# Optimization experiments

Hardware: AMD Instinct MI355X
Metric: run time of the kernel (lower is better)

## Reference

```python
import jax, jax.numpy as jnp
import numpy as np

# Mamba2 defaults (mamba_ssm): expand=2, headdim=64, d_conv=4, ngroups=1
D_MODEL, D_STATE, D_INNER, HEADDIM, D_CONV = 512, 64, 1024, 64, 4
NHEADS = D_INNER // HEADDIM  # 16
CONV_DIM = D_INNER + 2 * D_STATE  # 1152
D_IN_PROJ = 2 * D_INNER + 2 * D_STATE + NHEADS  # 2192
BATCH, SEQLEN = 2, 2048
RMS_EPS = 1.1920929e-07  # torch nn.RMSNorm eps=None -> fp32 machine eps
GNORM_EPS = 1e-5  # mamba_ssm RMSNormGated default


def _rms(t, w, eps):
    return t * jax.lax.rsqrt(jnp.mean(t * t, axis=-1, keepdims=True) + eps) * w


def _mamba2(u, in_w, conv_w, conv_b, dt_bias, A_log, Dp, gnorm_w, out_w):
    """Mamba2 block forward (ngroups=1). u: (b, l, d_model) -> (b, l, d_model)."""
    b, l, _ = u.shape
    zxbcdt = jnp.einsum('bld,ed->ble', u, in_w)  # (b, l, 2192)
    z = zxbcdt[..., :D_INNER]
    xBC = zxbcdt[..., D_INNER:D_INNER + CONV_DIM]
    dt = jax.nn.softplus(zxbcdt[..., -NHEADS:] + dt_bias)  # (b, l, h)
    # causal depthwise conv, kernel D_CONV, then SiLU
    xp = jnp.pad(xBC, ((0, 0), (D_CONV - 1, 0), (0, 0)))
    xBC = conv_b + sum(xp[:, i:i + l, :] * conv_w[:, i] for i in range(D_CONV))
    xBC = jax.nn.silu(xBC)
    x = xBC[..., :D_INNER].reshape(b, l, NHEADS, HEADDIM)
    Bm = xBC[..., D_INNER:D_INNER + D_STATE]  # (b, l, n)
    Cm = xBC[..., D_INNER + D_STATE:]         # (b, l, n)
    dA = jnp.exp(dt * (-jnp.exp(A_log)))      # (b, l, h), decay per head

    def step(h, inp):
        dA_t, dt_t, B_t, C_t, x_t = inp  # (b,h) (b,h) (b,n) (b,n) (b,h,p)
        h = h * dA_t[:, :, None, None] + jnp.einsum('bh,bhp,bn->bhpn', dt_t, x_t, B_t)
        y = jnp.einsum('bhpn,bn->bhp', h, C_t)
        return h, y

    h0 = jnp.zeros((b, NHEADS, HEADDIM, D_STATE), u.dtype)
    xs = (jnp.swapaxes(dA, 0, 1), jnp.swapaxes(dt, 0, 1), jnp.swapaxes(Bm, 0, 1),
          jnp.swapaxes(Cm, 0, 1), jnp.swapaxes(x, 0, 1))
    _, ys = jax.lax.scan(step, h0, xs)  # (l, b, h, p)
    y = jnp.swapaxes(ys, 0, 1) + x * Dp[None, None, :, None]
    y = y.reshape(b, l, D_INNER)
    # gated RMSNorm: norm(y * silu(z)) * weight
    y = y * jax.nn.silu(z)
    y = _rms(y, gnorm_w, GNORM_EPS)
    return jnp.einsum('bli,oi->blo', y, out_w)


def _layer(x, pos_emb, pixel_mask, norm_ssm_w, norm_ffn_w, ffn_w1, ffn_b1, ffn_w2, ffn_b2,
           f_in_w, f_conv_w, f_conv_b, f_dt_bias, f_A_log, f_D, f_gnorm_w, f_out_w,
           b_in_w, b_conv_w, b_conv_b, b_dt_bias, b_A_log, b_D, b_gnorm_w, b_out_w):
    si = _rms(x, norm_ssm_w, RMS_EPS) + pos_emb
    fwd = _mamba2(si, f_in_w, f_conv_w, f_conv_b, f_dt_bias, f_A_log, f_D, f_gnorm_w, f_out_w)
    bwd = jnp.flip(_mamba2(jnp.flip(si, 1), b_in_w, b_conv_w, b_conv_b, b_dt_bias,
                           b_A_log, b_D, b_gnorm_w, b_out_w), 1)
    ssm_out = (fwd + bwd) * pixel_mask[..., None]  # merge='add'
    x = x + ssm_out
    h = _rms(x, norm_ffn_w, RMS_EPS)
    h = jax.nn.gelu(h @ ffn_w1.T + ffn_b1, approximate=False)
    return x + (h @ ffn_w2.T + ffn_b2)


def setup_inputs() -> dict:
    key = jax.random.key(0)
    ks = jax.random.split(key, 16)
    f32 = jnp.float32
    inp = {}
    inp['x'] = jax.random.normal(ks[0], (BATCH, SEQLEN, D_MODEL), f32)
    inp['pos_emb'] = jax.random.normal(ks[1], (BATCH, SEQLEN, D_MODEL), f32) * 0.02
    inp['pixel_mask'] = jnp.ones((BATCH, SEQLEN), f32)
    inp['norm_ssm_w'] = jnp.ones((D_MODEL,), f32)
    inp['norm_ffn_w'] = jnp.ones((D_MODEL,), f32)
    d_ffn = 4 * D_MODEL
    inp['ffn_w1'] = jax.random.normal(ks[2], (d_ffn, D_MODEL), f32) * 0.02
    inp['ffn_b1'] = jnp.zeros((d_ffn,), f32)
    inp['ffn_w2'] = jax.random.normal(ks[3], (D_MODEL, d_ffn), f32) * 0.02
    inp['ffn_b2'] = jnp.zeros((D_MODEL,), f32)
    i = 4
    for pre in ('f', 'b'):
        inp[pre + '_in_w'] = jax.random.normal(ks[i], (D_IN_PROJ, D_MODEL), f32) * 0.02; i += 1
        inp[pre + '_conv_w'] = jax.random.uniform(ks[i], (CONV_DIM, D_CONV), f32, -0.5, 0.5); i += 1
        inp[pre + '_conv_b'] = jnp.zeros((CONV_DIM,), f32)
        dt0 = jnp.exp(jax.random.uniform(ks[i], (NHEADS,), f32) * (jnp.log(0.1) - jnp.log(0.001)) + jnp.log(0.001)); i += 1
        inp[pre + '_dt_bias'] = dt0 + jnp.log(-jnp.expm1(-dt0))  # inverse softplus
        inp[pre + '_A_log'] = jnp.log(jax.random.uniform(ks[i], (NHEADS,), f32, 1.0, 16.0)); i += 1
        inp[pre + '_D'] = jnp.ones((NHEADS,), f32)
        inp[pre + '_gnorm_w'] = jnp.ones((D_INNER,), f32)
        inp[pre + '_out_w'] = jax.random.normal(ks[i], (D_MODEL, D_INNER), f32) * 0.02; i += 1
    return inp


def reference(x, pos_emb, pixel_mask, norm_ssm_w, norm_ffn_w, ffn_w1, ffn_b1, ffn_w2, ffn_b2,
              f_in_w, f_conv_w, f_conv_b, f_dt_bias, f_A_log, f_D, f_gnorm_w, f_out_w,
              b_in_w, b_conv_w, b_conv_b, b_dt_bias, b_A_log, b_D, b_gnorm_w, b_out_w):
    return _layer(x, pos_emb, pixel_mask, norm_ssm_w, norm_ffn_w, ffn_w1, ffn_b1, ffn_w2, ffn_b2,
                  f_in_w, f_conv_w, f_conv_b, f_dt_bias, f_A_log, f_D, f_gnorm_w, f_out_w,
                  b_in_w, b_conv_w, b_conv_b, b_dt_bias, b_A_log, b_D, b_gnorm_w, b_out_w)
```

## Files before the change

### kernel.cpp

```cpp
#include <hip/hip_runtime.h>
#include <hip/hip_bf16.h>

typedef unsigned short u16;
typedef unsigned int u32;
typedef __bf16 bf16x8 __attribute__((ext_vector_type(8)));
typedef float f32x4 __attribute__((ext_vector_type(4)));

typedef __attribute__((address_space(1))) void gvoid_t;
typedef __attribute__((address_space(3))) void lvoid_t;
__device__ __forceinline__ void lds_cp16(void* lds, const void* g) {
    __builtin_amdgcn_global_load_lds((gvoid_t*)g, (lvoid_t*)lds, 16, 0, 0);
}

__device__ __forceinline__ float bf2f(u16 v) {
    u32 x = (u32)v << 16;
    return __builtin_bit_cast(float, x);
}
__device__ __forceinline__ u16 f2bf(float f) {
    return __builtin_bit_cast(u16, (__bf16)f);
}

__device__ __forceinline__ float wave_sum(float v) {
    #pragma unroll
    for (int o = 32; o > 0; o >>= 1) v += __shfl_xor(v, o);
    return v;
}

__device__ __forceinline__ void cvt4(const float* __restrict__ s, u16* __restrict__ d) {
    float4 v = *(const float4*)s;
    ushort4 o;
    o.x = f2bf(v.x); o.y = f2bf(v.y); o.z = f2bf(v.z); o.w = f2bf(v.w);
    *(ushort4*)d = o;
}

__global__ __launch_bounds__(256) void k_prep(
    const float* __restrict__ f_inw, const float* __restrict__ b_inw,
    const float* __restrict__ f_ow, const float* __restrict__ b_ow,
    const float* __restrict__ w1, const float* __restrict__ w2,
    u16* __restrict__ INWF, u16* __restrict__ INWB,
    u16* __restrict__ OWF, u16* __restrict__ OWB,
    u16* __restrict__ W1B, u16* __restrict__ W2B,
    const float* __restrict__ x, const float* __restrict__ pe,
    const float* __restrict__ wrms, u16* __restrict__ sib) {
    if (blockIdx.x < 5376) {
        int g = blockIdx.x * 256 + threadIdx.x;
        if (g < 294912) {
            int i = g * 4, n = i >> 9;
            if (n < 2192) cvt4(f_inw + i, INWF + i);
            else *(ushort4*)(INWF + i) = make_ushort4(0, 0, 0, 0);
            return;
        }
        g -= 294912;
        if (g < 294912) {
            int i = g * 4, n = i >> 9;
            if (n < 2192) cvt4(b_inw + i, INWB + i);
            else *(ushort4*)(INWB + i) = make_ushort4(0, 0, 0, 0);
            return;
        }
        g -= 294912;
        if (g < 131072) { cvt4(f_ow + g * 4, OWF + g * 4); return; }
        g -= 131072;
        if (g < 131072) { cvt4(b_ow + g * 4, OWB + g * 4); return; }
        g -= 131072;
        if (g < 262144) { cvt4(w1 + g * 4, W1B + g * 4); return; }
        g -= 262144;
        cvt4(w2 + g * 4, W2B + g * 4);
        return;
    }
    int row = (blockIdx.x - 5376) * 4 + (threadIdx.x >> 6);
    int lane = threadIdx.x & 63;
    size_t base = (size_t)row * 512 + lane * 4;
    float4 xa = *(const float4*)(x + base);
    float4 xb = *(const float4*)(x + base + 256);
    float ss = xa.x * xa.x + xa.y * xa.y + xa.z * xa.z + xa.w * xa.w
             + xb.x * xb.x + xb.y * xb.y + xb.z * xb.z + xb.w * xb.w;
    ss = wave_sum(ss);
    float sc = rsqrtf(ss * (1.f / 512.f) + 1.1920929e-07f);
    float4 pa = *(const float4*)(pe + base);
    float4 pb = *(const float4*)(pe + base + 256);
    float4 wa = *(const float4*)(wrms + lane * 4);
    float4 wb = *(const float4*)(wrms + lane * 4 + 256);
    ushort4 oa, obv;
    oa.x = f2bf(xa.x * sc * wa.x + pa.x);
    oa.y = f2bf(xa.y * sc * wa.y + pa.y);
    oa.z = f2bf(xa.z * sc * wa.z + pa.z);
    oa.w = f2bf(xa.w * sc * wa.w + pa.w);
    obv.x = f2bf(xb.x * sc * wb.x + pb.x);
    obv.y = f2bf(xb.y * sc * wb.y + pb.y);
    obv.z = f2bf(xb.z * sc * wb.z + pb.z);
    obv.w = f2bf(xb.w * sc * wb.w + pb.w);
    *(ushort4*)(sib + base) = oa;
    *(ushort4*)(sib + base + 256) = obv;
}

__global__ __launch_bounds__(256) void k_gemm_in(
    const u16* __restrict__ A, const u16* __restrict__ W0, const u16* __restrict__ W1,
    u16* __restrict__ Z0, u16* __restrict__ Z1,
    u16* __restrict__ XB0, u16* __restrict__ XB1) {
    const int z = blockIdx.z;
    const u16* W = z ? W1 : W0;
    u16* Z = z ? Z1 : Z0;
    u16* XB = z ? XB1 : XB0;
    const int K = 512;

    __shared__ __align__(16) u16 As[2][128 * 32];
    __shared__ __align__(16) u16 Bs[2][128 * 32];

    const int t = threadIdx.x;
    const int lane = t & 63;
    const int w = t >> 6;
    const int m0 = blockIdx.y * 128;
    const int n0 = blockIdx.x * 128;
    const int wm = (w >> 1) * 64;
    const int wn = (w & 1) * 64;
    const int fr = lane & 15;
    const int ksw = (((lane >> 4) ^ ((fr >> 1) & 3)) & 3) * 8;

    f32x4 acc[4][4];
    #pragma unroll
    for (int i = 0; i < 4; ++i)
        #pragma unroll
        for (int j = 0; j < 4; ++j) acc[i][j] = (f32x4){0.f, 0.f, 0.f, 0.f};

    auto STAGE = [&](int buf, int kt) {
        #pragma unroll
        for (int j = 0; j < 2; ++j) {
            int off16 = j * 256 + t;
            int row = off16 >> 2;
            int kc = (((off16 & 3) ^ ((row >> 1) & 3)) & 3) * 8;
            int gm = m0 + row;
            if (z) gm = (gm & ~2047) | (2047 - (gm & 2047));
            lds_cp16(As[buf] + off16 * 8, A + (size_t)gm * K + kt + kc);
            lds_cp16(Bs[buf] + off16 * 8, W + (size_t)(n0 + row) * K + kt + kc);
        }
    };

    STAGE(0, 0);
    __syncthreads();
    int cur = 0;
    for (int kt = 0; kt < K; kt += 32) {
        if (kt + 32 < K) STAGE(cur ^ 1, kt + 32);
        bf16x8 af[4], bfr[4];
        #pragma unroll
        for (int i = 0; i < 4; ++i) af[i] = *(const bf16x8*)(As[cur] + (wm + i * 16 + fr) * 32 + ksw);
        #pragma unroll
        for (int i = 0; i < 4; ++i) bfr[i] = *(const bf16x8*)(Bs[cur] + (wn + i * 16 + fr) * 32 + ksw);
        #pragma unroll
        for (int i = 0; i < 4; ++i)
            #pragma unroll
            for (int j = 0; j < 4; ++j)
                acc[i][j] = __builtin_amdgcn_mfma_f32_16x16x32_bf16(af[i], bfr[j], acc[i][j], 0, 0, 0);
        __syncthreads();
        cur ^= 1;
    }
    #pragma unroll
    for (int i = 0; i < 4; ++i) {
        int rbase = m0 + wm + i * 16 + (lane >> 4) * 4;
        #pragma unroll
        for (int j = 0; j < 4; ++j) {
            int c = n0 + wn + j * 16 + fr;
            #pragma unroll
            for (int r = 0; r < 4; ++r) {
                u16 v = f2bf(acc[i][j][r]);
                int m = rbase + r;
                if (c < 1024) Z[(size_t)m * 1024 + c] = v;
                else if (c < 2192) XB[(size_t)m * 1184 + (c - 1024)] = v;
            }
        }
    }
}

template <int EPI>
__global__ __launch_bounds__(256) void k_gemm128(
    const u16* __restrict__ A0, const u16* __restrict__ A1,
    const u16* __restrict__ W0, const u16* __restrict__ W1,
    u16* __restrict__ C0, u16* __restrict__ C1, int N, int K,
    const float* __restrict__ bias, const float* __restrict__ resid,
    float* __restrict__ outf) {
    const int z = blockIdx.z;
    const u16* A = z ? A1 : A0;
    const u16* W = z ? W1 : W0;
    u16* C = z ? C1 : C0;

    __shared__ __align__(16) u16 As[2][128 * 32];
    __shared__ __align__(16) u16 Bs[2][128 * 32];

    const int t = threadIdx.x;
    const int lane = t & 63;
    const int w = t >> 6;
    const int m0 = blockIdx.y * 128;
    const int n0 = blockIdx.x * 128;
    const int wm = (w >> 1) * 64;
    const int wn = (w & 1) * 64;
    const int fr = lane & 15;
    const int ksw = (((lane >> 4) ^ ((fr >> 1) & 3)) & 3) * 8;

    f32x4 acc[4][4];
    #pragma unroll
    for (int i = 0; i < 4; ++i)
        #pragma unroll
        for (int j = 0; j < 4; ++j) acc[i][j] = (f32x4){0.f, 0.f, 0.f, 0.f};

    auto STAGE = [&](int buf, int kt) {
        #pragma unroll
        for (int j = 0; j < 2; ++j) {
            int off16 = j * 256 + t;
            int row = off16 >> 2;
            int kc = (((off16 & 3) ^ ((row >> 1) & 3)) & 3) * 8;
            lds_cp16(As[buf] + off16 * 8, A + (size_t)(m0 + row) * K + kt + kc);
            lds_cp16(Bs[buf] + off16 * 8, W + (size_t)(n0 + row) * K + kt + kc);
        }
    };

    STAGE(0, 0);
    __syncthreads();
    int cur = 0;
    for (int kt = 0; kt < K; kt += 32) {
        if (kt + 32 < K) STAGE(cur ^ 1, kt + 32);
        bf16x8 af[4], bfr[4];
        #pragma unroll
        for (int i = 0; i < 4; ++i) af[i] = *(const bf16x8*)(As[cur] + (wm + i * 16 + fr) * 32 + ksw);
        #pragma unroll
        for (int i = 0; i < 4; ++i) bfr[i] = *(const bf16x8*)(Bs[cur] + (wn + i * 16 + fr) * 32 + ksw);
        #pragma unroll
        for (int i = 0; i < 4; ++i)
            #pragma unroll
            for (int j = 0; j < 4; ++j)
                acc[i][j] = __builtin_amdgcn_mfma_f32_16x16x32_bf16(af[i], bfr[j], acc[i][j], 0, 0, 0);
        __syncthreads();
        cur ^= 1;
    }
    #pragma unroll
    for (int i = 0; i < 4; ++i) {
        int rbase = m0 + wm + i * 16 + (lane >> 4) * 4;
        #pragma unroll
        for (int j = 0; j < 4; ++j) {
            int col = n0 + wn + j * 16 + fr;
            #pragma unroll
            for (int r = 0; r < 4; ++r) {
                int m = rbase + r;
                float v = acc[i][j][r];
                if (EPI == 0) {
                    C[(size_t)m * N + col] = f2bf(v);
                } else if (EPI == 1) {
                    float xg = v + bias[col];
                    C[(size_t)m * N + col] = f2bf(0.5f * xg * (1.f + erff(xg * 0.70710678118654752f)));
                } else {
                    outf[(size_t)m * N + col] = v + bias[col] + resid[(size_t)m * N + col];
                }
            }
        }
    }
}

template <int EPI>
__global__ __launch_bounds__(256) void k_gemm12864(
    const u16* __restrict__ A0, const u16* __restrict__ A1,
    const u16* __restrict__ W0, const u16* __restrict__ W1,
    u16* __restrict__ C0, u16* __restrict__ C1, int N, int K,
    const float* __restrict__ bias, const float* __restrict__ resid,
    float* __restrict__ outf) {
    const int z = blockIdx.z;
    const u16* A = z ? A1 : A0;
    const u16* W = z ? W1 : W0;
    u16* C = z ? C1 : C0;

    __shared__ __align__(16) u16 As[2][128 * 32];
    __shared__ __align__(16) u16 Bs[2][64 * 32];

    const int t = threadIdx.x;
    const int lane = t & 63;
    const int w = t >> 6;
    const int m0 = blockIdx.y * 128;
    const int n0 = blockIdx.x * 64;
    const int wm = w * 32;
    const int fr = lane & 15;
    const int ksw = (((lane >> 4) ^ ((fr >> 1) & 3)) & 3) * 8;

    f32x4 acc[2][4];
    #pragma unroll
    for (int i = 0; i < 2; ++i)
        #pragma unroll
        for (int j = 0; j < 4; ++j) acc[i][j] = (f32x4){0.f, 0.f, 0.f, 0.f};

    auto STAGE = [&](int buf, int kt) {
        #pragma unroll
        for (int j = 0; j < 2; ++j) {
            int off16 = j * 256 + t;
            int row = off16 >> 2;
            int kc = (((off16 & 3) ^ ((row >> 1) & 3)) & 3) * 8;
            lds_cp16(As[buf] + off16 * 8, A + (size_t)(m0 + row) * K + kt + kc);
        }
        int brow = t >> 2;
        int bkc = (((t & 3) ^ ((brow >> 1) & 3)) & 3) * 8;
        lds_cp16(Bs[buf] + t * 8, W + (size_t)(n0 + brow) * K + kt + bkc);
    };

    STAGE(0, 0);
    __syncthreads();
    int cur = 0;
    for (int kt = 0; kt < K; kt += 32) {
        if (kt + 32 < K) STAGE(cur ^ 1, kt + 32);
        bf16x8 af[2], bfr[4];
        #pragma unroll
        for (int i = 0; i < 2; ++i) af[i] = *(const bf16x8*)(As[cur] + (wm + i * 16 + fr) * 32 + ksw);
        #pragma unroll
        for (int j = 0; j < 4; ++j) bfr[j] = *(const bf16x8*)(Bs[cur] + (j * 16 + fr) * 32 + ksw);
        #pragma unroll
        for (int i = 0; i < 2; ++i)
            #pragma unroll
            for (int j = 0; j < 4; ++j)
                acc[i][j] = __builtin_amdgcn_mfma_f32_16x16x32_bf16(af[i], bfr[j], acc[i][j], 0, 0, 0);
        __syncthreads();
        cur ^= 1;
    }
    #pragma unroll
    for (int i = 0; i < 2; ++i) {
        int rbase = m0 + wm + i * 16 + (lane >> 4) * 4;
        #pragma unroll
        for (int j = 0; j < 4; ++j) {
            int col = n0 + j * 16 + fr;
            #pragma unroll
            for (int r = 0; r < 4; ++r) {
                int m = rbase + r;
                float v = acc[i][j][r];
                if (EPI == 0) {
                    C[(size_t)m * N + col] = f2bf(v);
                } else if (EPI == 1) {
                    float xg = v + bias[col];
                    C[(size_t)m * N + col] = f2bf(0.5f * xg * (1.f + erff(xg * 0.70710678118654752f)));
                } else {
                    outf[(size_t)m * N + col] = v + bias[col] + resid[(size_t)m * N + col];
                }
            }
        }
    }
}

template <int EPI>
__global__ __launch_bounds__(256) void k_gemm64(
    const u16* __restrict__ A0, const u16* __restrict__ A1,
    const u16* __restrict__ W0, const u16* __restrict__ W1,
    u16* __restrict__ C0, u16* __restrict__ C1, int N, int K,
    const float* __restrict__ bias, const float* __restrict__ resid,
    float* __restrict__ outf) {
    const int z = blockIdx.z;
    const u16* A = z ? A1 : A0;
    const u16* W = z ? W1 : W0;
    u16* C = z ? C1 : C0;

    __shared__ __align__(16) u16 As[2][64 * 32];
    __shared__ __align__(16) u16 Bs[2][64 * 32];

    const int t = threadIdx.x;
    const int lane = t & 63;
    const int w = t >> 6;
    const int m0 = blockIdx.y * 64;
    const int n0 = blockIdx.x * 64;
    const int wm = (w >> 1) * 32;
    const int wn = (w & 1) * 32;
    const int fr = lane & 15;
    const int ksw = (((lane >> 4) ^ ((fr >> 1) & 3)) & 3) * 8;

    f32x4 acc[2][2];
    #pragma unroll
    for (int i = 0; i < 2; ++i)
        #pragma unroll
        for (int j = 0; j < 2; ++j) acc[i][j] = (f32x4){0.f, 0.f, 0.f, 0.f};

    const int srow = t >> 2;
    const int skc = (((t & 3) ^ ((srow >> 1) & 3)) & 3) * 8;
    auto STAGE = [&](int buf, int kt) {
        lds_cp16(As[buf] + t * 8, A + (size_t)(m0 + srow) * K + kt + skc);
        lds_cp16(Bs[buf] + t * 8, W + (size_t)(n0 + srow) * K + kt + skc);
    };

    STAGE(0, 0);
    __syncthreads();
    int cur = 0;
    for (int kt = 0; kt < K; kt += 32) {
        if (kt + 32 < K) STAGE(cur ^ 1, kt + 32);
        bf16x8 af[2], bfr[2];
        #pragma unroll
        for (int i = 0; i < 2; ++i) af[i] = *(const bf16x8*)(As[cur] + (wm + i * 16 + fr) * 32 + ksw);
        #pragma unroll
        for (int j = 0; j < 2; ++j) bfr[j] = *(const bf16x8*)(Bs[cur] + (wn + j * 16 + fr) * 32 + ksw);
        #pragma unroll
        for (int i = 0; i < 2; ++i)
            #pragma unroll
            for (int j = 0; j < 2; ++j)
                acc[i][j] = __builtin_amdgcn_mfma_f32_16x16x32_bf16(af[i], bfr[j], acc[i][j], 0, 0, 0);
        __syncthreads();
        cur ^= 1;
    }
    #pragma unroll
    for (int i = 0; i < 2; ++i) {
        int rbase = m0 + wm + i * 16 + (lane >> 4) * 4;
        #pragma unroll
        for (int j = 0; j < 2; ++j) {
            int col = n0 + wn + j * 16 + fr;
            #pragma unroll
            for (int r = 0; r < 4; ++r) {
                int m = rbase + r;
                float v = acc[i][j][r];
                if (EPI == 0) {
                    C[(size_t)m * N + col] = f2bf(v);
                } else if (EPI == 1) {
                    float xg = v + bias[col];
                    C[(size_t)m * N + col] = f2bf(0.5f * xg * (1.f + erff(xg * 0.70710678118654752f)));
                } else {
                    outf[(size_t)m * N + col] = v + bias[col] + resid[(size_t)m * N + col];
                }
            }
        }
    }
}

__global__ __launch_bounds__(160) void k_conv(
    const u16* __restrict__ xb0, const u16* __restrict__ xb1,
    const float* __restrict__ cw0, const float* __restrict__ cb0,
    const float* __restrict__ dtb0, const float* __restrict__ al0,
    const float* __restrict__ cw1, const float* __restrict__ cb1,
    const float* __restrict__ dtb1, const float* __restrict__ al1,
    u16* __restrict__ xc0, u16* __restrict__ xc1,
    float* __restrict__ dtO0, float* __restrict__ dAO0,
    float* __restrict__ dtO1, float* __restrict__ dAO1) {
    int g = blockIdx.x;
    int dir = g >> 9;
    int row0 = (g & 511) * 8;
    const u16* xb = dir ? xb1 : xb0;
    const float* cw = dir ? cw1 : cw0;
    const float* cb = dir ? cb1 : cb0;
    const float* dtb = dir ? dtb1 : dtb0;
    const float* al = dir ? al1 : al0;
    u16* xc = dir ? xc1 : xc0;
    float* dtO = dir ? dtO1 : dtO0;
    float* dAO = dir ? dAO1 : dAO0;
    int tl0 = row0 & 2047;
    int rbatch = row0 - tl0;
    int t = threadIdx.x;
    if (t < 144) {
        int col = t * 8;
        float cwa[8][4];
        #pragma unroll
        for (int j = 0; j < 8; ++j) {
            float4 c4 = *(const float4*)(cw + (col + j) * 4);
            cwa[j][0] = c4.x; cwa[j][1] = c4.y; cwa[j][2] = c4.z; cwa[j][3] = c4.w;
        }
        float cbv[8];
        float4 cb0v = *(const float4*)(cb + col);
        float4 cb1v = *(const float4*)(cb + col + 4);
        cbv[0] = cb0v.x; cbv[1] = cb0v.y; cbv[2] = cb0v.z; cbv[3] = cb0v.w;
        cbv[4] = cb1v.x; cbv[5] = cb1v.y; cbv[6] = cb1v.z; cbv[7] = cb1v.w;
        uint4 win[4];
        win[0] = win[1] = win[2] = make_uint4(0, 0, 0, 0);
        #pragma unroll
        for (int i = 0; i < 3; ++i) {
            int tt = tl0 - 3 + i;
            if (tt >= 0) win[i] = *(const uint4*)(xb + (size_t)(rbatch + tt) * 1184 + col);
        }
        for (int s = 0; s < 8; ++s) {
            win[3] = *(const uint4*)(xb + (size_t)(rbatch + tl0 + s) * 1184 + col);
            const u16* w0 = (const u16*)&win[0];
            const u16* w1 = (const u16*)&win[1];
            const u16* w2 = (const u16*)&win[2];
            const u16* w3 = (const u16*)&win[3];
            u16 ov[8];
            #pragma unroll
            for (int j = 0; j < 8; ++j) {
                float a = cbv[j] + bf2f(w0[j]) * cwa[j][0] + bf2f(w1[j]) * cwa[j][1]
                        + bf2f(w2[j]) * cwa[j][2] + bf2f(w3[j]) * cwa[j][3];
                ov[j] = f2bf(a / (1.f + expf(-a)));
            }
            *(uint4*)(xc + (size_t)(row0 + s) * 1152 + col) = *(const uint4*)ov;
            win[0] = win[1]; win[1] = win[2]; win[2] = win[3];
        }
    } else if (t < 160) {
        int hh = t - 144;
        float nal = -expf(al[hh]);
        float dtbv = dtb[hh];
        for (int s = 0; s < 8; ++s) {
            int row = row0 + s;
            float v = bf2f(xb[(size_t)row * 1184 + 1152 + hh]) + dtbv;
            float sp = (v > 20.f) ? v : log1pf(expf(v));
            dtO[row * 16 + hh] = sp;
            dAO[row * 16 + hh] = nal * sp;
        }
    }
}

__global__ __launch_bounds__(256) void k_ssd_state(
    const u16* __restrict__ xc0, const float* __restrict__ dt0, const float* __restrict__ ld0,
    const u16* __restrict__ xc1, const float* __restrict__ dt1, const float* __restrict__ ld1,
    float* __restrict__ S, float* __restrict__ Aprod) {
    int blk = blockIdx.x;
    int c = blk & 31, h = (blk >> 5) & 15, b = (blk >> 9) & 1, dir = blk >> 10;
    const u16* xc = dir ? xc1 : xc0;
    const float* dtp = dir ? dt1 : dt0;
    const float* ldp = dir ? ld1 : ld0;
    const int t = threadIdx.x, w = t >> 6, lane = t & 63;
    const int fr = lane & 15, fk = (lane >> 4) * 8;

    __shared__ __align__(16) u16 sBt[64 * 72];
    __shared__ __align__(16) u16 sXp[64 * 72];
    __shared__ float ssc[64];
    size_t row0 = (size_t)b * 2048 + c * 64;

    if (t < 64) {
        float v = ldp[(row0 + t) * 16 + h];
        float dtv = dtp[(row0 + t) * 16 + h];
        #pragma unroll
        for (int o = 1; o < 64; o <<= 1) {
            float u = __shfl_up(v, o);
            if (lane >= o) v += u;
        }
        float last = __shfl(v, 63);
        ssc[t] = dtv * expf(last - v);
        if (t == 63) Aprod[blk] = expf(v);
    }
    __syncthreads();
    #pragma unroll
    for (int i2 = t; i2 < 512; i2 += 256) {
        int r = i2 >> 3, e8 = (i2 & 7) * 8;
        size_t rb = (row0 + r) * 1152;
        uint4 bv = *(const uint4*)(xc + rb + 1024 + e8);
        uint4 xv = *(const uint4*)(xc + rb + h * 64 + e8);
        const u16* bs = (const u16*)&bv;
        const u16* xs = (const u16*)&xv;
        float sc = ssc[r];
        #pragma unroll
        for (int j = 0; j < 8; ++j) {
            sBt[(e8 + j) * 72 + r] = bs[j];
            sXp[(e8 + j) * 72 + r] = f2bf(bf2f(xs[j]) * sc);
        }
    }
    __syncthreads();

    f32x4 acc[4];
    #pragma unroll
    for (int j = 0; j < 4; ++j) acc[j] = (f32x4){0.f, 0.f, 0.f, 0.f};
    #pragma unroll
    for (int k0 = 0; k0 < 64; k0 += 32) {
        bf16x8 a = *(const bf16x8*)(sBt + (w * 16 + fr) * 72 + k0 + fk);
        #pragma unroll
        for (int j = 0; j < 4; ++j) {
            bf16x8 bb = *(const bf16x8*)(sXp + (j * 16 + fr) * 72 + k0 + fk);
            acc[j] = __builtin_amdgcn_mfma_f32_16x16x32_bf16(a, bb, acc[j], 0, 0, 0);
        }
    }
    float* Sb = S + (size_t)blk * 4096;
    int nb = w * 16 + (lane >> 4) * 4;
    #pragma unroll
    for (int j = 0; j < 4; ++j) {
        int p = j * 16 + fr;
        *(f32x4*)(Sb + p * 64 + nb) = acc[j];
    }
}

__global__ __launch_bounds__(256) void k_scan_carry(float* __restrict__ S,
                                                    const float* __restrict__ Aprod) {
    int g = blockIdx.x;
    int blk = g >> 4;
    int e = (g & 15) * 256 + threadIdx.x;
    size_t base = (size_t)blk * 32 * 4096 + e;
    float sv[32];
    #pragma unroll
    for (int c = 0; c < 32; ++c) sv[c] = S[base + (size_t)c * 4096];
    float ap[32];
    #pragma unroll
    for (int c = 0; c < 32; ++c) ap[c] = Aprod[blk * 32 + c];
    float h = 0.f;
    #pragma unroll
    for (int c = 0; c < 32; ++c) {
        S[base + (size_t)c * 4096] = h;
        h = ap[c] * h + sv[c];
    }
}

__global__ __launch_bounds__(256) void k_ssd_y(
    const u16* __restrict__ xc0, const float* __restrict__ dt0, const float* __restrict__ ld0,
    const float* __restrict__ Dv0, u16* __restrict__ y0,
    const u16* __restrict__ xc1, const float* __restrict__ dt1, const float* __restrict__ ld1,
    const float* __restrict__ Dv1, u16* __restrict__ y1,
    const float* __restrict__ S) {
    int blk = blockIdx.x;
    int c = blk & 31, h = (blk >> 5) & 15, b = (blk >> 9) & 1, dir = blk >> 10;
    const u16* xc = dir ? xc1 : xc0;
    const float* dtp = dir ? dt1 : dt0;
    const float* ldp = dir ? ld1 : ld0;
    u16* y = dir ? y1 : y0;
    const float Dh = (dir ? Dv1 : Dv0)[h];
    const int t = threadIdx.x, w = t >> 6, lane = t & 63;
    const int fr = lane & 15, fk = (lane >> 4) * 8;

    __shared__ __align__(16) u16 sB[64 * 72];
    __shared__ __align__(16) u16 sC[64 * 72];
    __shared__ __align__(16) u16 sXp[64 * 72];
    __shared__ __align__(16) u16 sHi[64 * 72];
    __shared__ __align__(16) u16 sLo[64 * 72];
    __shared__ __align__(16) u16 sGl[64 * 72];
    __shared__ float scl[64], sdt[64];
    size_t row0 = (size_t)b * 2048 + c * 64;

    if (t < 64) {
        float v = ldp[(row0 + t) * 16 + h];
        float dtv = dtp[(row0 + t) * 16 + h];
        #pragma unroll
        for (int o = 1; o < 64; o <<= 1) {
            float u = __shfl_up(v, o);
            if (lane >= o) v += u;
        }
        scl[t] = v;
        sdt[t] = dtv;
    }
    __syncthreads();
    #pragma unroll
    for (int i2 = t; i2 < 512; i2 += 256) {
        int r = i2 >> 3, e8 = (i2 & 7) * 8;
        size_t rb = (row0 + r) * 1152;
        *(uint4*)(sB + r * 72 + e8) = *(const uint4*)(xc + rb + 1024 + e8);
        *(uint4*)(sC + r * 72 + e8) = *(const uint4*)(xc + rb + 1088 + e8);
        uint4 xv = *(const uint4*)(xc + rb + h * 64 + e8);
        const u16* xs = (const u16*)&xv;
        float dtv = sdt[r];
        #pragma unroll
        for (int j = 0; j < 8; ++j) sXp[(e8 + j) * 72 + r] = f2bf(bf2f(xs[j]) * dtv);
    }
    #pragma unroll
    for (int i4 = t; i4 < 1024; i4 += 256) {
        int p = i4 >> 4, n4 = (i4 & 15) * 4;
        float4 hv = *(const float4*)(S + (size_t)blk * 4096 + p * 64 + n4);
        ushort4 hi4, lo4;
        hi4.x = f2bf(hv.x); lo4.x = f2bf(hv.x - bf2f(hi4.x));
        hi4.y = f2bf(hv.y); lo4.y = f2bf(hv.y - bf2f(hi4.y));
        hi4.z = f2bf(hv.z); lo4.z = f2bf(hv.z - bf2f(hi4.z));
        hi4.w = f2bf(hv.w); lo4.w = f2bf(hv.w - bf2f(hi4.w));
        *(ushort4*)(sHi + p * 72 + n4) = hi4;
        *(ushort4*)(sLo + p * 72 + n4) = lo4;
    }
    __syncthreads();

    f32x4 g[4], acc2[4];
    #pragma unroll
    for (int j = 0; j < 4; ++j) { g[j] = (f32x4){0.f,0.f,0.f,0.f}; acc2[j] = (f32x4){0.f,0.f,0.f,0.f}; }
    #pragma unroll
    for (int k0 = 0; k0 < 64; k0 += 32) {
        bf16x8 a = *(const bf16x8*)(sC + (w * 16 + fr) * 72 + k0 + fk);
        #pragma unroll
        for (int j = 0; j < 4; ++j) {
            bf16x8 bb = *(const bf16x8*)(sB + (j * 16 + fr) * 72 + k0 + fk);
            g[j] = __builtin_amdgcn_mfma_f32_16x16x32_bf16(a, bb, g[j], 0, 0, 0);
            bf16x8 bh = *(const bf16x8*)(sHi + (j * 16 + fr) * 72 + k0 + fk);
            acc2[j] = __builtin_amdgcn_mfma_f32_16x16x32_bf16(a, bh, acc2[j], 0, 0, 0);
            bf16x8 bl = *(const bf16x8*)(sLo + (j * 16 + fr) * 72 + k0 + fk);
            acc2[j] = __builtin_amdgcn_mfma_f32_16x16x32_bf16(a, bl, acc2[j], 0, 0, 0);
        }
    }
    #pragma unroll
    for (int j = 0; j < 4; ++j) {
        int r = j * 16 + fr;
        #pragma unroll
        for (int reg = 0; reg < 4; ++reg) {
            int s = w * 16 + (lane >> 4) * 4 + reg;
            float val = (r <= s) ? expf(scl[s] - scl[r]) * g[j][reg] : 0.f;
            sGl[s * 72 + r] = f2bf(val);
        }
    }
    __syncthreads();

    f32x4 acc1[4];
    #pragma unroll
    for (int j = 0; j < 4; ++j) acc1[j] = (f32x4){0.f, 0.f, 0.f, 0.f};
    #pragma unroll
    for (int k0 = 0; k0 < 64; k0 += 32) {
        bf16x8 a = *(const bf16x8*)(sGl + (w * 16 + fr) * 72 + k0 + fk);
        #pragma unroll
        for (int j = 0; j < 4; ++j) {
            bf16x8 bb = *(const bf16x8*)(sXp + (j * 16 + fr) * 72 + k0 + fk);
            acc1[j] = __builtin_amdgcn_mfma_f32_16x16x32_bf16(a, bb, acc1[j], 0, 0, 0);
        }
    }
    #pragma unroll
    for (int reg = 0; reg < 4; ++reg) {
        int s = w * 16 + (lane >> 4) * 4 + reg;
        float es = expf(scl[s]);
        size_t yrb = (row0 + s) * 1024 + h * 64;
        size_t xrb = (row0 + s) * 1152 + h * 64;
        #pragma unroll
        for (int j = 0; j < 4; ++j) {
            int p = j * 16 + fr;
            float xv = bf2f(xc[xrb + p]);
            y[yrb + p] = f2bf(acc1[j][reg] + es * acc2[j][reg] + xv * Dh);
        }
    }
}

__global__ __launch_bounds__(256) void k_gnorm(
    const u16* __restrict__ y0, const u16* __restrict__ z0,
    const float* __restrict__ gw0, u16* __restrict__ o0,
    const u16* __restrict__ y1, const u16* __restrict__ z1,
    const float* __restrict__ gw1, u16* __restrict__ o1) {
    int idx = blockIdx.x * 4 + (threadIdx.x >> 6);
    int dir = idx >> 12, row = idx & 4095;
    int lane = threadIdx.x & 63;
    const u16* y = dir ? y1 : y0;
    const u16* zp = dir ? z1 : z0;
    const float* gw = dir ? gw1 : gw0;
    u16* o = dir ? o1 : o0;
    size_t base = (size_t)row * 1024 + lane * 8;
    uint4 ya = *(const uint4*)(y + base);
    uint4 yb = *(const uint4*)(y + base + 512);
    uint4 za = *(const uint4*)(zp + base);
    uint4 zb = *(const uint4*)(zp + base + 512);
    const u16* yap = (const u16*)&ya;
    const u16* ybp = (const u16*)&yb;
    const u16* zap = (const u16*)&za;
    const u16* zbp = (const u16*)&zb;
    float v[16];
    float ss = 0.f;
    #pragma unroll
    for (int j = 0; j < 8; ++j) {
        float zf = bf2f(zap[j]);
        v[j] = bf2f(yap[j]) * (zf / (1.f + expf(-zf)));
        ss += v[j] * v[j];
    }
    #pragma unroll
    for (int j = 0; j < 8; ++j) {
        float zf = bf2f(zbp[j]);
        v[8 + j] = bf2f(ybp[j]) * (zf / (1.f + expf(-zf)));
        ss += v[8 + j] * v[8 + j];
    }
    ss = wave_sum(ss);
    float sc = rsqrtf(ss * (1.f / 1024.f) + 1e-5f);
    float4 g0 = *(const float4*)(gw + lane * 8);
    float4 g1 = *(const float4*)(gw + lane * 8 + 4);
    float4 g2 = *(const float4*)(gw + 512 + lane * 8);
    float4 g3 = *(const float4*)(gw + 512 + lane * 8 + 4);
    const float* gp0 = (const float*)&g0;
    const float* gp1 = (const float*)&g1;
    const float* gp2 = (const float*)&g2;
    const float* gp3 = (const float*)&g3;
    u16 oa[8], obv[8];
    #pragma unroll
    for (int j = 0; j < 4; ++j) {
        oa[j] = f2bf(v[j] * sc * gp0[j]);
        oa[4 + j] = f2bf(v[4 + j] * sc * gp1[j]);
        obv[j] = f2bf(v[8 + j] * sc * gp2[j]);
        obv[4 + j] = f2bf(v[12 + j] * sc * gp3[j]);
    }
    *(uint4*)(o + base) = *(const uint4*)oa;
    *(uint4*)(o + base + 512) = *(const uint4*)obv;
}

__global__ __launch_bounds__(256) void k_add_rms(
    const float* __restrict__ x, const u16* __restrict__ of,
    const u16* __restrict__ ob, const float* __restrict__ mask,
    const float* __restrict__ wrms,
    float* __restrict__ x2, u16* __restrict__ o) {
    int row = blockIdx.x * 4 + (threadIdx.x >> 6);
    int lane = threadIdx.x & 63;
    int bb = row >> 11, tl = row & 2047;
    size_t fb = (size_t)((bb << 11) + (2047 - tl)) * 512;
    float m = mask[row];
    size_t base = (size_t)row * 512 + lane * 4;
    size_t fo = fb + lane * 4;
    float4 xa = *(const float4*)(x + base);
    float4 xb = *(const float4*)(x + base + 256);
    ushort4 fa = *(const ushort4*)(of + base);
    ushort4 fbv = *(const ushort4*)(of + base + 256);
    ushort4 ba = *(const ushort4*)(ob + fo);
    ushort4 bbv = *(const ushort4*)(ob + fo + 256);
    float va[4], vb[4];
    va[0] = xa.x + (bf2f(fa.x) + bf2f(ba.x)) * m;
    va[1] = xa.y + (bf2f(fa.y) + bf2f(ba.y)) * m;
    va[2] = xa.z + (bf2f(fa.z) + bf2f(ba.z)) * m;
    va[3] = xa.w + (bf2f(fa.w) + bf2f(ba.w)) * m;
    vb[0] = xb.x + (bf2f(fbv.x) + bf2f(bbv.x)) * m;
    vb[1] = xb.y + (bf2f(fbv.y) + bf2f(bbv.y)) * m;
    vb[2] = xb.z + (bf2f(fbv.z) + bf2f(bbv.z)) * m;
    vb[3] = xb.w + (bf2f(fbv.w) + bf2f(bbv.w)) * m;
    *(float4*)(x2 + base) = (float4){va[0], va[1], va[2], va[3]};
    *(float4*)(x2 + base + 256) = (float4){vb[0], vb[1], vb[2], vb[3]};
    float ss = va[0]*va[0] + va[1]*va[1] + va[2]*va[2] + va[3]*va[3]
             + vb[0]*vb[0] + vb[1]*vb[1] + vb[2]*vb[2] + vb[3]*vb[3];
    ss = wave_sum(ss);
    float sc = rsqrtf(ss * (1.f / 512.f) + 1.1920929e-07f);
    float4 wa = *(const float4*)(wrms + lane * 4);
    float4 wb = *(const float4*)(wrms + lane * 4 + 256);
    ushort4 oa, obv;
    oa.x = f2bf(va[0] * sc * wa.x);
    oa.y = f2bf(va[1] * sc * wa.y);
    oa.z = f2bf(va[2] * sc * wa.z);
    oa.w = f2bf(va[3] * sc * wa.w);
    obv.x = f2bf(vb[0] * sc * wb.x);
    obv.y = f2bf(vb[1] * sc * wb.y);
    obv.z = f2bf(vb[2] * sc * wb.z);
    obv.w = f2bf(vb[3] * sc * wb.w);
    *(ushort4*)(o + base) = oa;
    *(ushort4*)(o + base + 256) = obv;
}

extern "C" void kernel_launch(void* const* d_in, const int* in_sizes, int n_in,
                              void* d_out, int out_size, void* d_ws, size_t ws_size,
                              hipStream_t stream) {
    const float* x = (const float*)d_in[0];
    const float* pe = (const float*)d_in[1];
    const float* mask = (const float*)d_in[2];
    const float* nsw = (const float*)d_in[3];
    const float* nfw = (const float*)d_in[4];
    const float* w1 = (const float*)d_in[5];
    const float* b1 = (const float*)d_in[6];
    const float* w2 = (const float*)d_in[7];
    const float* b2 = (const float*)d_in[8];
    const float* f_inw = (const float*)d_in[9];
    const float* f_cw = (const float*)d_in[10];
    const float* f_cb = (const float*)d_in[11];
    const float* f_dtb = (const float*)d_in[12];
    const float* f_al = (const float*)d_in[13];
    const float* f_D = (const float*)d_in[14];
    const float* f_gw = (const float*)d_in[15];
    const float* f_ow = (const float*)d_in[16];
    const float* b_inw = (const float*)d_in[17];
    const float* b_cw = (const float*)d_in[18];
    const float* b_cb = (const float*)d_in[19];
    const float* b_dtb = (const float*)d_in[20];
    const float* b_al = (const float*)d_in[21];
    const float* b_D = (const float*)d_in[22];
    const float* b_gw = (const float*)d_in[23];
    const float* b_ow = (const float*)d_in[24];
    float* out = (float*)d_out;

    char* ws = (char*)d_ws;
    u16* Z0   = (u16*)(ws + 0);
    u16* Z1   = (u16*)(ws + 8388608);
    u16* XB0  = (u16*)(ws + 16777216);
    u16* XB1  = (u16*)(ws + 26476544);
    u16* INWF = (u16*)(ws + 36175872);
    u16* INWB = (u16*)(ws + 38535168);
    u16* SIB  = (u16*)(ws + 40894464);
    u16* XC0  = (u16*)(ws + 36175872);
    u16* XC1  = (u16*)(ws + 45613056);
    float* dtF = (float*)(ws + 55050240);
    float* dAF = (float*)(ws + 55312384);
    float* dtB = (float*)(ws + 55574528);
    float* dAB = (float*)(ws + 55836672);
    u16* Y0   = (u16*)(ws + 16777216);
    u16* Y1   = (u16*)(ws + 25165824);
    u16* YG0  = (u16*)(ws + 36175872);
    u16* YG1  = (u16*)(ws + 44564480);
    u16* OP0  = (u16*)(ws + 0);
    u16* OP1  = (u16*)(ws + 4194304);
    float* X2 = (float*)(ws + 8388608);
    u16* X2B  = (u16*)(ws + 0);
    u16* HACT = (u16*)(ws + 16777216);
    u16* OWF = (u16*)(ws + 56098816);
    u16* OWB = (u16*)(ws + 57147392);
    u16* W1B = (u16*)(ws + 58195968);
    u16* W2B = (u16*)(ws + 60293120);
    float* SBUF = (float*)(ws + 62390272);
    float* APR  = (float*)(ws + 95944704);

    k_prep<<<6400, 256, 0, stream>>>(f_inw, b_inw, f_ow, b_ow, w1, w2,
                                     INWF, INWB, OWF, OWB, W1B, W2B,
                                     x, pe, nsw, SIB);
    k_gemm_in<<<dim3(18, 32, 2), 256, 0, stream>>>(SIB, INWF, INWB, Z0, Z1, XB0, XB1);
    k_conv<<<1024, 160, 0, stream>>>(XB0, XB1, f_cw, f_cb, f_dtb, f_al,
                                     b_cw, b_cb, b_dtb, b_al,
                                     XC0, XC1, dtF, dAF, dtB, dAB);
    k_ssd_state<<<2048, 256, 0, stream>>>(XC0, dtF, dAF, XC1, dtB, dAB, SBUF, APR);
    k_scan_carry<<<1024, 256, 0, stream>>>(SBUF, APR);
    k_ssd_y<<<2048, 256, 0, stream>>>(XC0, dtF, dAF, f_D, Y0,
                                      XC1, dtB, dAB, b_D, Y1, SBUF);
    k_gnorm<<<2048, 256, 0, stream>>>(Y0, Z0, f_gw, YG0, Y1, Z1, b_gw, YG1);
    k_gemm12864<0><<<dim3(8, 32, 2), 256, 0, stream>>>(YG0, YG1, OWF, OWB, OP0, OP1, 512, 1024,
                                                       nullptr, nullptr, nullptr);
    k_add_rms<<<1024, 256, 0, stream>>>(x, OP0, OP1, mask, nfw, X2, X2B);
    k_gemm128<1><<<dim3(16, 32, 1), 256, 0, stream>>>(X2B, X2B, W1B, W1B, HACT, HACT, 2048, 512,
                                                      b1, nullptr, nullptr);
    k_gemm64<2><<<dim3(8, 64, 1), 256, 0, stream>>>(HACT, HACT, W2B, W2B, nullptr, nullptr,
                                                    512, 2048, b2, X2, out);
}
```

Measured before the change: 328.7 us.

## Triple-buffer GEMM K-loop with explicit vmcnt waits and one barrier per step

Converts the double-buffered LDS staging in all four GEMM kernels to a three-stage ring with two tiles prefetched ahead. Each step uses an explicit s_waitcnt on outstanding global-to-LDS loads plus a single s_barrier, replacing the __syncthreads that drained every load. This is meant to hide global load latency behind MFMA work. It raises LDS use per block, which may lower occupancy. The in-projection epilogue is also split into Z and XB branches per block to drop per-element column checks.

```diff
diff --git a/kernel.cpp b/kernel.cpp
--- a/kernel.cpp
+++ b/kernel.cpp
@@ -103,8 +103,8 @@
     u16* XB = z ? XB1 : XB0;
     const int K = 512;
 
-    __shared__ __align__(16) u16 As[2][128 * 32];
-    __shared__ __align__(16) u16 Bs[2][128 * 32];
+    __shared__ __align__(16) u16 As[3][128 * 32];
+    __shared__ __align__(16) u16 Bs[3][128 * 32];
 
     const int t = threadIdx.x;
     const int lane = t & 63;
@@ -135,36 +135,59 @@
         }
     };
 
+    const int NS = 16;
     STAGE(0, 0);
-    __syncthreads();
-    int cur = 0;
-    for (int kt = 0; kt < K; kt += 32) {
-        if (kt + 32 < K) STAGE(cur ^ 1, kt + 32);
+    STAGE(1, 32);
+    asm volatile("s_waitcnt vmcnt(4)" ::: "memory");
+    __builtin_amdgcn_s_barrier();
+    __builtin_amdgcn_sched_barrier(0);
+    int b0 = 0, b1 = 1, b2 = 2;
+    for (int i = 0; i < NS; ++i) {
+        if (i + 2 < NS) STAGE(b2, (i + 2) << 5);
+        const u16* Ac = As[b0];
+        const u16* Bc = Bs[b0];
         bf16x8 af[4], bfr[4];
         #pragma unroll
-        for (int i = 0; i < 4; ++i) af[i] = *(const bf16x8*)(As[cur] + (wm + i * 16 + fr) * 32 + ksw);
-        #pragma unroll
-        for (int i = 0; i < 4; ++i) bfr[i] = *(const bf16x8*)(Bs[cur] + (wn + i * 16 + fr) * 32 + ksw);
-        #pragma unroll
-        for (int i = 0; i < 4; ++i)
+        for (int ii = 0; ii < 4; ++ii) af[ii] = *(const bf16x8*)(Ac + (wm + ii * 16 + fr) * 32 + ksw);
+        #pragma unroll
+        for (int ii = 0; ii < 4; ++ii) bfr[ii] = *(const bf16x8*)(Bc + (wn + ii * 16 + fr) * 32 + ksw);
+        #pragma unroll
+        for (int ii = 0; ii < 4; ++ii)
             #pragma unroll
-            for (int j = 0; j < 4; ++j)
-                acc[i][j] = __builtin_amdgcn_mfma_f32_16x16x32_bf16(af[i], bfr[j], acc[i][j], 0, 0, 0);
-        __syncthreads();
-        cur ^= 1;
-    }
-    #pragma unroll
-    for (int i = 0; i < 4; ++i) {
-        int rbase = m0 + wm + i * 16 + (lane >> 4) * 4;
-        #pragma unroll
-        for (int j = 0; j < 4; ++j) {
-            int c = n0 + wn + j * 16 + fr;
+            for (int jj = 0; jj < 4; ++jj)
+                acc[ii][jj] = __builtin_amdgcn_mfma_f32_16x16x32_bf16(af[ii], bfr[jj], acc[ii][jj], 0, 0, 0);
+        if (i + 1 < NS) {
+            if (i + 2 < NS) asm volatile("s_waitcnt vmcnt(4) lgkmcnt(0)" ::: "memory");
+            else            asm volatile("s_waitcnt vmcnt(0) lgkmcnt(0)" ::: "memory");
+            __builtin_amdgcn_s_barrier();
+            __builtin_amdgcn_sched_barrier(0);
+        }
+        int bt = b0; b0 = b1; b1 = b2; b2 = bt;
+    }
+    if (n0 < 1024) {
+        #pragma unroll
+        for (int i = 0; i < 4; ++i) {
+            int rbase = m0 + wm + i * 16 + (lane >> 4) * 4;
             #pragma unroll
-            for (int r = 0; r < 4; ++r) {
-                u16 v = f2bf(acc[i][j][r]);
-                int m = rbase + r;
-                if (c < 1024) Z[(size_t)m * 1024 + c] = v;
-                else if (c < 2192) XB[(size_t)m * 1184 + (c - 1024)] = v;
+            for (int j = 0; j < 4; ++j) {
+                int c = n0 + wn + j * 16 + fr;
+                #pragma unroll
+                for (int r = 0; r < 4; ++r)
+                    Z[(size_t)(rbase + r) * 1024 + c] = f2bf(acc[i][j][r]);
+            }
+        }
+    } else {
+        #pragma unroll
+        for (int i = 0; i < 4; ++i) {
+            int rbase = m0 + wm + i * 16 + (lane >> 4) * 4;
+            #pragma unroll
+            for (int j = 0; j < 4; ++j) {
+                int cx = n0 - 1024 + wn + j * 16 + fr;
+                if (cx < 1168) {
+                    #pragma unroll
+                    for (int r = 0; r < 4; ++r)
+                        XB[(size_t)(rbase + r) * 1184 + cx] = f2bf(acc[i][j][r]);
+                }
             }
         }
     }
@@ -182,8 +205,8 @@
     const u16* W = z ? W1 : W0;
     u16* C = z ? C1 : C0;
 
-    __shared__ __align__(16) u16 As[2][128 * 32];
-    __shared__ __align__(16) u16 Bs[2][128 * 32];
+    __shared__ __align__(16) u16 As[3][128 * 32];
+    __shared__ __align__(16) u16 Bs[3][128 * 32];
 
     const int t = threadIdx.x;
     const int lane = t & 63;
@@ -212,23 +235,34 @@
         }
     };
 
+    const int NS = K >> 5;
     STAGE(0, 0);
-    __syncthreads();
-    int cur = 0;
-    for (int kt = 0; kt < K; kt += 32) {
-        if (kt + 32 < K) STAGE(cur ^ 1, kt + 32);
+    STAGE(1, 32);
+    asm volatile("s_waitcnt vmcnt(4)" ::: "memory");
+    __builtin_amdgcn_s_barrier();
+    __builtin_amdgcn_sched_barrier(0);
+    int b0 = 0, b1 = 1, b2 = 2;
+    for (int i = 0; i < NS; ++i) {
+        if (i + 2 < NS) STAGE(b2, (i + 2) << 5);
+        const u16* Ac = As[b0];
+        const u16* Bc = Bs[b0];
         bf16x8 af[4], bfr[4];
         #pragma unroll
-        for (int i = 0; i < 4; ++i) af[i] = *(const bf16x8*)(As[cur] + (wm + i * 16 + fr) * 32 + ksw);
-        #pragma unroll
-        for (int i = 0; i < 4; ++i) bfr[i] = *(const bf16x8*)(Bs[cur] + (wn + i * 16 + fr) * 32 + ksw);
-        #pragma unroll
-        for (int i = 0; i < 4; ++i)
+        for (int ii = 0; ii < 4; ++ii) af[ii] = *(const bf16x8*)(Ac + (wm + ii * 16 + fr) * 32 + ksw);
+        #pragma unroll
+        for (int ii = 0; ii < 4; ++ii) bfr[ii] = *(const bf16x8*)(Bc + (wn + ii * 16 + fr) * 32 + ksw);
+        #pragma unroll
+        for (int ii = 0; ii < 4; ++ii)
             #pragma unroll
-            for (int j = 0; j < 4; ++j)
-                acc[i][j] = __builtin_amdgcn_mfma_f32_16x16x32_bf16(af[i], bfr[j], acc[i][j], 0, 0, 0);
-        __syncthreads();
-        cur ^= 1;
+            for (int jj = 0; jj < 4; ++jj)
+                acc[ii][jj] = __builtin_amdgcn_mfma_f32_16x16x32_bf16(af[ii], bfr[jj], acc[ii][jj], 0, 0, 0);
+        if (i + 1 < NS) {
+            if (i + 2 < NS) asm volatile("s_waitcnt vmcnt(4) lgkmcnt(0)" ::: "memory");
+            else            asm volatile("s_waitcnt vmcnt(0) lgkmcnt(0)" ::: "memory");
+            __builtin_amdgcn_s_barrier();
+            __builtin_amdgcn_sched_barrier(0);
+        }
+        int bt = b0; b0 = b1; b1 = b2; b2 = bt;
     }
     #pragma unroll
     for (int i = 0; i < 4; ++i) {
@@ -265,8 +299,8 @@
     const u16* W = z ? W1 : W0;
     u16* C = z ? C1 : C0;
 
-    __shared__ __align__(16) u16 As[2][128 * 32];
-    __shared__ __align__(16) u16 Bs[2][64 * 32];
+    __shared__ __align__(16) u16 As[3][128 * 32];
+    __shared__ __align__(16) u16 Bs[3][64 * 32];
 
     const int t = threadIdx.x;
     const int lane = t & 63;
@@ -296,23 +330,34 @@
         lds_cp16(Bs[buf] + t * 8, W + (size_t)(n0 + brow) * K + kt + bkc);
     };
 
+    const int NS = K >> 5;
     STAGE(0, 0);
-    __syncthreads();
-    int cur = 0;
-    for (int kt = 0; kt < K; kt += 32) {
-        if (kt + 32 < K) STAGE(cur ^ 1, kt + 32);
+    STAGE(1, 32);
+    asm volatile("s_waitcnt vmcnt(3)" ::: "memory");
+    __builtin_amdgcn_s_barrier();
+    __builtin_amdgcn_sched_barrier(0);
+    int b0 = 0, b1 = 1, b2 = 2;
+    for (int i = 0; i < NS; ++i) {
+        if (i + 2 < NS) STAGE(b2, (i + 2) << 5);
+        const u16* Ac = As[b0];
+        const u16* Bc = Bs[b0];
         bf16x8 af[2], bfr[4];
         #pragma unroll
-        for (int i = 0; i < 2; ++i) af[i] = *(const bf16x8*)(As[cur] + (wm + i * 16 + fr) * 32 + ksw);
-        #pragma unroll
-        for (int j = 0; j < 4; ++j) bfr[j] = *(const bf16x8*)(Bs[cur] + (j * 16 + fr) * 32 + ksw);
-        #pragma unroll
-        for (int i = 0; i < 2; ++i)
+        for (int ii = 0; ii < 2; ++ii) af[ii] = *(const bf16x8*)(Ac + (wm + ii * 16 + fr) * 32 + ksw);
+        #pragma unroll
+        for (int jj = 0; jj < 4; ++jj) bfr[jj] = *(const bf16x8*)(Bc + (jj * 16 + fr) * 32 + ksw);
+        #pragma unroll
+        for (int ii = 0; ii < 2; ++ii)
             #pragma unroll
-            for (int j = 0; j < 4; ++j)
-                acc[i][j] = __builtin_amdgcn_mfma_f32_16x16x32_bf16(af[i], bfr[j], acc[i][j], 0, 0, 0);
-        __syncthreads();
-        cur ^= 1;
+            for (int jj = 0; jj < 4; ++jj)
+                acc[ii][jj] = __builtin_amdgcn_mfma_f32_16x16x32_bf16(af[ii], bfr[jj], acc[ii][jj], 0, 0, 0);
+        if (i + 1 < NS) {
+            if (i + 2 < NS) asm volatile("s_waitcnt vmcnt(3) lgkmcnt(0)" ::: "memory");
+            else            asm volatile("s_waitcnt vmcnt(0) lgkmcnt(0)" ::: "memory");
+            __builtin_amdgcn_s_barrier();
+            __builtin_amdgcn_sched_barrier(0);
+        }
+        int bt = b0; b0 = b1; b1 = b2; b2 = bt;
     }
     #pragma unroll
     for (int i = 0; i < 2; ++i) {
@@ -349,8 +394,8 @@
     const u16* W = z ? W1 : W0;
     u16* C = z ? C1 : C0;
 
-    __shared__ __align__(16) u16 As[2][64 * 32];
-    __shared__ __align__(16) u16 Bs[2][64 * 32];
+    __shared__ __align__(16) u16 As[3][64 * 32];
+    __shared__ __align__(16) u16 Bs[3][64 * 32];
 
     const int t = threadIdx.x;
     const int lane = t & 63;
@@ -375,23 +420,34 @@
         lds_cp16(Bs[buf] + t * 8, W + (size_t)(n0 + srow) * K + kt + skc);
     };
 
+    const int NS = K >> 5;
     STAGE(0, 0);
-    __syncthreads();
-    int cur = 0;
-    for (int kt = 0; kt < K; kt += 32) {
-        if (kt + 32 < K) STAGE(cur ^ 1, kt + 32);
+    STAGE(1, 32);
+    asm volatile("s_waitcnt vmcnt(2)" ::: "memory");
+    __builtin_amdgcn_s_barrier();
+    __builtin_amdgcn_sched_barrier(0);
+    int b0 = 0, b1 = 1, b2 = 2;
+    for (int i = 0; i < NS; ++i) {
+        if (i + 2 < NS) STAGE(b2, (i + 2) << 5);
+        const u16* Ac = As[b0];
+        const u16* Bc = Bs[b0];
         bf16x8 af[2], bfr[2];
         #pragma unroll
-        for (int i = 0; i < 2; ++i) af[i] = *(const bf16x8*)(As[cur] + (wm + i * 16 + fr) * 32 + ksw);
-        #pragma unroll
-        for (int j = 0; j < 2; ++j) bfr[j] = *(const bf16x8*)(Bs[cur] + (wn + j * 16 + fr) * 32 + ksw);
-        #pragma unroll
-        for (int i = 0; i < 2; ++i)
+        for (int ii = 0; ii < 2; ++ii) af[ii] = *(const bf16x8*)(Ac + (wm + ii * 16 + fr) * 32 + ksw);
+        #pragma unroll
+        for (int jj = 0; jj < 2; ++jj) bfr[jj] = *(const bf16x8*)(Bc + (wn + jj * 16 + fr) * 32 + ksw);
+        #pragma unroll
+        for (int ii = 0; ii < 2; ++ii)
             #pragma unroll
-            for (int j = 0; j < 2; ++j)
-                acc[i][j] = __builtin_amdgcn_mfma_f32_16x16x32_bf16(af[i], bfr[j], acc[i][j], 0, 0, 0);
-        __syncthreads();
-        cur ^= 1;
+            for (int jj = 0; jj < 2; ++jj)
+                acc[ii][jj] = __builtin_amdgcn_mfma_f32_16x16x32_bf16(af[ii], bfr[jj], acc[ii][jj], 0, 0, 0);
+        if (i + 1 < NS) {
+            if (i + 2 < NS) asm volatile("s_waitcnt vmcnt(2) lgkmcnt(0)" ::: "memory");
+            else            asm volatile("s_waitcnt vmcnt(0) lgkmcnt(0)" ::: "memory");
+            __builtin_amdgcn_s_barrier();
+            __builtin_amdgcn_sched_barrier(0);
+        }
+        int bt = b0; b0 = b1; b1 = b2; b2 = bt;
     }
     #pragma unroll
     for (int i = 0; i < 2; ++i) {
```

Result: no change. 327.0 us (-0.5%).
